# Optimization experiments

Hardware: AMD Instinct MI355X
Metric: run time of the kernel (lower is better)

The kernel has to match this reference:

```python
import jax, jax.numpy as jnp
import numpy as np

N_NODES = 50000
N_EDGES = 800000
D_IN = 128
D_OUT = 128


def setup_inputs() -> dict:
    key = jax.random.key(0)
    k1, k2, k3, k4, k5 = jax.random.split(key, 5)
    x = jax.random.normal(k1, (N_NODES, D_IN), dtype=jnp.float32)
    edge_index = jax.random.randint(k2, (2, N_EDGES), 0, N_NODES, dtype=jnp.int64)
    # PyG SAGEConv params: lin_l (neighbors, with bias), lin_r (root, no bias)
    scale = 1.0 / np.sqrt(D_IN)
    W_l = jax.random.uniform(k3, (D_OUT, D_IN), dtype=jnp.float32, minval=-scale, maxval=scale)
    b_l = jax.random.uniform(k4, (D_OUT,), dtype=jnp.float32, minval=-scale, maxval=scale)
    W_r = jax.random.uniform(k5, (D_OUT, D_IN), dtype=jnp.float32, minval=-scale, maxval=scale)
    return {"x": x, "edge_index": edge_index, "W_l": W_l, "b_l": b_l, "W_r": W_r}


def reference(x, edge_index, W_l, b_l, W_r):
    src, dst = edge_index[0], edge_index[1]
    # mean aggregation of neighbor (source) features into destination nodes
    msg = x[src]  # [E, D_IN]
    agg_sum = jax.ops.segment_sum(msg, dst, num_segments=N_NODES)  # [N, D_IN]
    deg = jax.ops.segment_sum(jnp.ones((N_EDGES,), dtype=x.dtype), dst, num_segments=N_NODES)
    agg = agg_sum / jnp.maximum(deg, 1.0)[:, None]  # isolated nodes -> 0
    # out = lin_l(agg) + lin_r(x); ReLU from SAGE_NET wrapper (active=True)
    out = agg @ W_l.T + b_l + x @ W_r.T
    return jax.nn.relu(out)
```

## Files before the change

### kernel.cpp

```cpp
#include <hip/hip_runtime.h>
#include <hip/hip_bf16.h>

#define NNODES 50000
#define NEDGES 800000
#define DD 128
#define NPART 8
#define PSIZE 6250
#define CAP 64
#define FILL_B 25000
#define XCV_B 6250
#define WB_B 64
#define WP2 68

typedef unsigned int u32;
typedef unsigned short u16;
typedef short bf16x8 __attribute__((ext_vector_type(8)));
typedef float f32x4 __attribute__((ext_vector_type(4)));
typedef float f32x2 __attribute__((ext_vector_type(2)));

#if defined(__has_builtin)
#if __has_builtin(__builtin_amdgcn_cvt_pk_f32_fp8)
#define HAVE_HW_FP8 1
#endif
#endif

union U4B8 {
    uint4 u;
    bf16x8 b;
};

__device__ __forceinline__ u32 f2b(float f) {
    u32 u = __float_as_uint(f);
    u32 rounding = 0x7fffu + ((u >> 16) & 1u);
    return (u + rounding) >> 16;
}

__device__ __forceinline__ u32 f2e4m3(float f) {
    u32 u = __float_as_uint(f);
    u32 s = (u >> 31) << 7;
    u32 mag = u & 0x7fffffffu;
    if (mag < 0x3c800000u) return s;
    u32 t = mag + 0x0007FFFFu + ((mag >> 20) & 1u);
    u32 e = (t >> 23) - 120u;
    u32 m = (t >> 20) & 7u;
    if (e > 15u || (e == 15u && m == 7u)) { e = 15u; m = 6u; }
    return s | (e << 3) | m;
}

__device__ __forceinline__ void fp8x4_acc(u32 v, float& a0, float& a1,
                                          float& a2, float& a3) {
#ifdef HAVE_HW_FP8
    f32x2 lo = __builtin_amdgcn_cvt_pk_f32_fp8((int)v, false);
    f32x2 hi = __builtin_amdgcn_cvt_pk_f32_fp8((int)v, true);
    a0 += lo.x;
    a1 += lo.y;
    a2 += hi.x;
    a3 += hi.y;
#else
#pragma unroll
    for (int b = 0; b < 4; ++b) {
        u32 byte = (v >> (8 * b)) & 0xffu;
        u32 f = ((byte >> 7) << 31) | ((((byte >> 3) & 15u) + 120u) << 23) |
                ((byte & 7u) << 20);
        float val = (byte & 0x78u) ? __uint_as_float(f) : 0.f;
        if (b == 0) a0 += val;
        else if (b == 1) a1 += val;
        else if (b == 2) a2 += val;
        else a3 += val;
    }
#endif
}

__global__ __launch_bounds__(256) void work_k(
    const int* __restrict__ ei, u32* __restrict__ deg,
    u16* __restrict__ slots16, const float* __restrict__ x,
    u32* __restrict__ xb, u32* __restrict__ xq,
    const float* __restrict__ Wl, const float* __restrict__ Wr,
    u32* __restrict__ wb) {
    const int b = blockIdx.x, tid = threadIdx.x;
    if (b < FILL_B) {
        u32 part = (u32)b & (NPART - 1);
        u32 e = ((u32)b >> 3) * 256u + tid;
        int dst = ei[NEDGES + e];
        if ((u32)(dst - part * PSIZE) < (u32)PSIZE) {
            u32 pos = atomicAdd(deg + dst, 1u);
            if (pos < CAP) slots16[(size_t)dst * CAP + pos] = (u16)ei[e];
        }
    } else if (b < FILL_B + XCV_B) {
        int i = (b - FILL_B) * 256 + tid;
        float4 v = ((const float4*)x)[i];
        uint2 o;
        o.x = f2b(v.x) | (f2b(v.y) << 16);
        o.y = f2b(v.z) | (f2b(v.w) << 16);
        ((uint2*)xb)[i] = o;
        xq[i] = f2e4m3(v.x) | (f2e4m3(v.y) << 8) | (f2e4m3(v.z) << 16) |
                (f2e4m3(v.w) << 24);
    } else {
        int idx = (b - FILL_B - XCV_B) * 256 + tid;
        int o = idx >> 7, c = idx & 127, k0 = 2 * c;
        const float* src = (k0 < DD) ? (Wl + o * DD + k0) : (Wr + o * DD + (k0 - DD));
        wb[idx] = f2b(src[0]) | (f2b(src[1]) << 16);
    }
}

__global__ __launch_bounds__(512, 4) void sage_fused_k(
    const u32* __restrict__ xq, const u16* __restrict__ slots16,
    const u32* __restrict__ deg, const u32* __restrict__ xb,
    const u32* __restrict__ wb, const float* __restrict__ bl,
    float* __restrict__ out) {
    __shared__ u32 w2[DD * WP2];
    __shared__ u32 agg_lds[128 * WP2];
    __shared__ float sbias[DD];
    const int tid = threadIdx.x;
    const int row0 = blockIdx.x * 128;
    const int wave = tid >> 6, lane = tid & 63;
    const int m = lane & 15, quad = lane >> 4;

    for (int r = tid >> 5; r < DD; r += 16) {
        int c2 = (tid & 31) * 2;
        *(uint2*)&w2[r * WP2 + c2] = *(const uint2*)&wb[r * DD + c2];
    }
    if (tid < DD) sbias[tid] = bl[tid];

    uint4 af_x[4];
    {
        int r = row0 + wave * 16 + m;
        r = r < NNODES ? r : NNODES - 1;
        const u32* xrow = xb + (size_t)r * 64;
#pragma unroll
        for (int ks = 0; ks < 4; ++ks)
            af_x[ks] = *(const uint4*)&xrow[ks * 16 + quad * 4];
    }

    const u32 half = lane >> 5;
    const u32 q = lane & 31u;
    const u32 nbase = (u32)(row0 + wave * 16);
    u32 d = (nbase < NNODES) ? deg[nbase] : 0u;
    u32 sv = (nbase < NNODES) ? (u32)slots16[(size_t)nbase * CAP + lane] : 0u;
    for (int i = 0; i < 16; ++i) {
        u32 d_n = 0u, sv_n = 0u;
        if (i < 15) {
            u32 nn = nbase + (u32)i + 1u;
            if (nn < NNODES) {
                d_n = deg[nn];
                sv_n = (u32)slots16[(size_t)nn * CAP + lane];
            }
        }
        u32 cnt = min(d, (u32)CAP);
        float a0 = 0.f, a1 = 0.f, a2 = 0.f, a3 = 0.f;
        u32 j = 0;
        for (; j + 16 <= cnt; j += 16) {
            u32 v[8];
#pragma unroll
            for (int p = 0; p < 8; ++p) {
                u32 sA = __shfl(sv, (int)(j + 2 * p), 64);
                u32 sB = __shfl(sv, (int)(j + 2 * p + 1), 64);
                u32 s = half ? sB : sA;
                v[p] = xq[(size_t)s * 32 + q];
            }
#pragma unroll
            for (int p = 0; p < 8; ++p) fp8x4_acc(v[p], a0, a1, a2, a3);
        }
        for (; j + 2 <= cnt; j += 2) {
            u32 sA = __shfl(sv, (int)j, 64);
            u32 sB = __shfl(sv, (int)(j + 1), 64);
            u32 s = half ? sB : sA;
            fp8x4_acc(xq[(size_t)s * 32 + q], a0, a1, a2, a3);
        }
        if (j < cnt) {
            u32 sA = __shfl(sv, (int)j, 64);
            u32 v = xq[(size_t)sA * 32 + q];
            if (!half) fp8x4_acc(v, a0, a1, a2, a3);
        }
        a0 += __shfl_xor(a0, 32, 64);
        a1 += __shfl_xor(a1, 32, 64);
        a2 += __shfl_xor(a2, 32, 64);
        a3 += __shfl_xor(a3, 32, 64);
        if (lane < 32) {
            float inv = 1.0f / fmaxf((float)d, 1.0f);
            uint2 o;
            o.x = f2b(a0 * inv) | (f2b(a1 * inv) << 16);
            o.y = f2b(a2 * inv) | (f2b(a3 * inv) << 16);
            *(uint2*)&agg_lds[(wave * 16 + i) * WP2 + q * 2] = o;
        }
        d = d_n;
        sv = sv_n;
    }
    __syncthreads();

    f32x4 acc[8];
#pragma unroll
    for (int nt = 0; nt < 8; ++nt) acc[nt] = (f32x4){0.f, 0.f, 0.f, 0.f};

#pragma unroll
    for (int ks = 0; ks < 4; ++ks) {
        U4B8 af;
        af.u = *(const uint4*)&agg_lds[(wave * 16 + m) * WP2 + ks * 16 + quad * 4];
#pragma unroll
        for (int nt = 0; nt < 8; ++nt) {
            U4B8 bf;
            bf.u = *(const uint4*)&w2[(nt * 16 + m) * WP2 + ks * 16 + quad * 4];
            acc[nt] = __builtin_amdgcn_mfma_f32_16x16x32_bf16(af.b, bf.b,
                                                              acc[nt], 0, 0, 0);
        }
    }
    __syncthreads();
    for (int r = tid >> 5; r < DD; r += 16) {
        int c2 = (tid & 31) * 2;
        *(uint2*)&w2[r * WP2 + c2] = *(const uint2*)&wb[r * DD + 64 + c2];
    }
    __syncthreads();

#pragma unroll
    for (int ks = 0; ks < 4; ++ks) {
        U4B8 af;
        af.u = af_x[ks];
#pragma unroll
        for (int nt = 0; nt < 8; ++nt) {
            U4B8 bf;
            bf.u = *(const uint4*)&w2[(nt * 16 + m) * WP2 + ks * 16 + quad * 4];
            acc[nt] = __builtin_amdgcn_mfma_f32_16x16x32_bf16(af.b, bf.b,
                                                              acc[nt], 0, 0, 0);
        }
    }

#pragma unroll
    for (int nt = 0; nt < 8; ++nt) {
        int col = nt * 16 + m;
        float b = sbias[col];
#pragma unroll
        for (int r_ = 0; r_ < 4; ++r_) {
            int row = row0 + wave * 16 + quad * 4 + r_;
            if (row < NNODES)
                out[(size_t)row * DD + col] = fmaxf(acc[nt][r_] + b, 0.f);
        }
    }
}

__global__ __launch_bounds__(256) void scatter_k(
    const float* __restrict__ x, const int* __restrict__ ei,
    float* __restrict__ agg, u32* __restrict__ deg) {
    u32 gid = blockIdx.x * 256u + threadIdx.x;
    u32 edge = gid >> 6;
    u32 lane = gid & 63u;
    if (edge >= NEDGES) return;
    int src = ei[edge];
    int dst = ei[NEDGES + edge];
    float2 v = ((const float2*)(x + (size_t)src * DD))[lane];
    float* p = agg + (size_t)dst * DD + lane * 2u;
    unsafeAtomicAdd(p, v.x);
    unsafeAtomicAdd(p + 1, v.y);
    if (lane == 0) atomicAdd(deg + dst, 1u);
}

__global__ __launch_bounds__(256) void mean_k(
    float* __restrict__ agg, const u32* __restrict__ deg) {
    u32 gid = blockIdx.x * 256u + threadIdx.x;
    u32 node = gid >> 6;
    u32 lane = gid & 63u;
    if (node >= NNODES) return;
    float inv = 1.0f / fmaxf((float)deg[node], 1.0f);
    float2* p = (float2*)(agg + (size_t)node * DD) + lane;
    float2 v = *p;
    *p = make_float2(v.x * inv, v.y * inv);
}

__global__ __launch_bounds__(256) void lin_l_k(
    float* __restrict__ agg,
    const float* __restrict__ Wl, const float* __restrict__ bl) {
    __shared__ u32 WT[DD * 65];
    __shared__ float rows[4 * DD];
    __shared__ float sbias[DD];
    const int tid = threadIdx.x;
    {
        u16* WTs = (u16*)WT;
        for (int i = tid; i < DD * DD; i += 256) {
            int o = i >> 7, k = i & 127;
            WTs[k * 130 + o] = (u16)f2b(Wl[i]);
        }
        if (tid < DD) sbias[tid] = bl[tid];
    }
    __syncthreads();
    const int h = tid & 63;
    const int nl = tid >> 6;
    for (int base = blockIdx.x * 4; base < NNODES; base += gridDim.x * 4) {
        ((float2*)rows)[tid] =
            ((const float2*)(agg + (size_t)(base + (tid >> 6)) * DD))[tid & 63];
        __syncthreads();
        float acc0 = sbias[2 * h], acc1 = sbias[2 * h + 1];
#pragma unroll
        for (int k = 0; k < DD; ++k) {
            float a = rows[nl * DD + k];
            u32 w2 = WT[k * 65 + h];
            acc0 = fmaf(a, __uint_as_float(w2 << 16), acc0);
            acc1 = fmaf(a, __uint_as_float(w2 & 0xffff0000u), acc1);
        }
        __syncthreads();
        ((float2*)(agg + (size_t)(base + nl) * DD))[h] = make_float2(acc0, acc1);
    }
}

__global__ __launch_bounds__(256) void lin_r_k(
    float* __restrict__ io, const float* __restrict__ x,
    const float* __restrict__ Wr) {
    __shared__ u32 WT[DD * 65];
    __shared__ float rows[4 * DD];
    const int tid = threadIdx.x;
    {
        u16* WTs = (u16*)WT;
        for (int i = tid; i < DD * DD; i += 256) {
            int o = i >> 7, k = i & 127;
            WTs[k * 130 + o] = (u16)f2b(Wr[i]);
        }
    }
    __syncthreads();
    const int h = tid & 63;
    const int nl = tid >> 6;
    for (int base = blockIdx.x * 4; base < NNODES; base += gridDim.x * 4) {
        ((float2*)rows)[tid] =
            ((const float2*)(x + (size_t)(base + (tid >> 6)) * DD))[tid & 63];
        __syncthreads();
        float2 t2 = ((const float2*)(io + (size_t)(base + nl) * DD))[h];
        float acc0 = t2.x, acc1 = t2.y;
#pragma unroll
        for (int k = 0; k < DD; ++k) {
            float a = rows[nl * DD + k];
            u32 w2 = WT[k * 65 + h];
            acc0 = fmaf(a, __uint_as_float(w2 << 16), acc0);
            acc1 = fmaf(a, __uint_as_float(w2 & 0xffff0000u), acc1);
        }
        acc0 = fmaxf(acc0, 0.f);
        acc1 = fmaxf(acc1, 0.f);
        __syncthreads();
        ((float2*)(io + (size_t)(base + nl) * DD))[h] = make_float2(acc0, acc1);
    }
}

extern "C" void kernel_launch(void* const* d_in, const int* in_sizes, int n_in,
                              void* d_out, int out_size, void* d_ws, size_t ws_size,
                              hipStream_t stream) {
    const float* x  = (const float*)d_in[0];
    const int*   ei = (const int*)d_in[1];
    const float* Wl = (const float*)d_in[2];
    const float* bl = (const float*)d_in[3];
    const float* Wr = (const float*)d_in[4];

    u32* deg     = (u32*)d_ws;
    u16* slots16 = (u16*)(deg + NNODES);
    u32* wb      = (u32*)d_ws + NNODES + (size_t)NNODES * (CAP / 2);
    u32* xb      = wb + 16384;
    u32* xq      = xb + (size_t)NNODES * 64;
    const size_t need =
        ((size_t)NNODES * (1 + CAP / 2 + 64 + 32) + 16384) * 4;

    if (ws_size >= need) {
        hipMemsetAsync(deg, 0, (size_t)NNODES * sizeof(u32), stream);
        work_k<<<FILL_B + XCV_B + WB_B, 256, 0, stream>>>(
            ei, deg, slots16, x, xb, xq, Wl, Wr, wb);
        sage_fused_k<<<(NNODES + 127) / 128, 512, 0, stream>>>(
            xq, slots16, deg, xb, wb, bl, (float*)d_out);
    } else {
        float* agg = (float*)d_out;
        hipMemsetAsync(d_out, 0, (size_t)NNODES * DD * sizeof(float), stream);
        hipMemsetAsync(d_ws, 0, (size_t)NNODES * sizeof(u32), stream);
        scatter_k<<<(NEDGES * 64) / 256, 256, 0, stream>>>(x, ei, agg, deg);
        mean_k<<<(NNODES * 64 + 255) / 256, 256, 0, stream>>>(agg, deg);
        lin_l_k<<<1024, 256, 0, stream>>>(agg, Wl, bl);
        lin_r_k<<<1024, 256, 0, stream>>>(agg, x, Wr);
    }
}
```

Measured before the change: 177.4 us.

## Interleave fill and convert blocks and halve rows per fused block

```diff
diff --git a/kernel.cpp b/kernel.cpp
--- a/kernel.cpp
+++ b/kernel.cpp
@@ -7,9 +7,8 @@
 #define NPART 8
 #define PSIZE 6250
 #define CAP 64
-#define FILL_B 25000
-#define XCV_B 6250
-#define WB_B 64
+#define NGROUPS 3910
+#define WK_B (NGROUPS * 8 + 64)
 #define WP2 68
 
 typedef unsigned int u32;
@@ -78,43 +77,54 @@
     const float* __restrict__ Wl, const float* __restrict__ Wr,
     u32* __restrict__ wb) {
     const int b = blockIdx.x, tid = threadIdx.x;
-    if (b < FILL_B) {
-        u32 part = (u32)b & (NPART - 1);
-        u32 e = ((u32)b >> 3) * 256u + tid;
-        int dst = ei[NEDGES + e];
-        if ((u32)(dst - part * PSIZE) < (u32)PSIZE) {
-            u32 pos = atomicAdd(deg + dst, 1u);
-            if (pos < CAP) slots16[(size_t)dst * CAP + pos] = (u16)ei[e];
-        }
-    } else if (b < FILL_B + XCV_B) {
-        int i = (b - FILL_B) * 256 + tid;
-        float4 v = ((const float4*)x)[i];
-        uint2 o;
-        o.x = f2b(v.x) | (f2b(v.y) << 16);
-        o.y = f2b(v.z) | (f2b(v.w) << 16);
-        ((uint2*)xb)[i] = o;
-        xq[i] = f2e4m3(v.x) | (f2e4m3(v.y) << 8) | (f2e4m3(v.z) << 16) |
-                (f2e4m3(v.w) << 24);
+    if (b < NGROUPS * 8) {
+        const u32 g = (u32)b >> 3, r8 = (u32)b & 7u;
+        const u32 gm = g % 5u, gq = g / 5u;
+        if (gm < 4u) {
+            u32 fg = gq * 4u + gm;
+            if (fg < 3125u) {
+                u32 e = fg * 256u + tid;
+                int dst = ei[NEDGES + e];
+                if ((u32)(dst - r8 * PSIZE) < (u32)PSIZE) {
+                    u32 pos = atomicAdd(deg + dst, 1u);
+                    if (pos < CAP) slots16[(size_t)dst * CAP + pos] = (u16)ei[e];
+                }
+            }
+        } else {
+            u32 xi = gq * 8u + r8;
+            if (xi < 6250u) {
+                int i = (int)xi * 256 + tid;
+                float4 v = ((const float4*)x)[i];
+                uint2 o;
+                o.x = f2b(v.x) | (f2b(v.y) << 16);
+                o.y = f2b(v.z) | (f2b(v.w) << 16);
+                ((uint2*)xb)[i] = o;
+                xq[i] = f2e4m3(v.x) | (f2e4m3(v.y) << 8) | (f2e4m3(v.z) << 16) |
+                        (f2e4m3(v.w) << 24);
+            }
+        }
     } else {
-        int idx = (b - FILL_B - XCV_B) * 256 + tid;
+        int idx = (b - NGROUPS * 8) * 256 + tid;
         int o = idx >> 7, c = idx & 127, k0 = 2 * c;
         const float* src = (k0 < DD) ? (Wl + o * DD + k0) : (Wr + o * DD + (k0 - DD));
         wb[idx] = f2b(src[0]) | (f2b(src[1]) << 16);
     }
 }
 
-__global__ __launch_bounds__(512, 4) void sage_fused_k(
+__global__ __launch_bounds__(512, 6) void sage_fused_k(
     const u32* __restrict__ xq, const u16* __restrict__ slots16,
     const u32* __restrict__ deg, const u32* __restrict__ xb,
     const u32* __restrict__ wb, const float* __restrict__ bl,
     float* __restrict__ out) {
     __shared__ u32 w2[DD * WP2];
-    __shared__ u32 agg_lds[128 * WP2];
+    __shared__ u32 agg_lds[64 * WP2];
     __shared__ float sbias[DD];
     const int tid = threadIdx.x;
-    const int row0 = blockIdx.x * 128;
+    const int row0 = blockIdx.x * 64;
     const int wave = tid >> 6, lane = tid & 63;
     const int m = lane & 15, quad = lane >> 4;
+    const int rw = wave & 3;
+    const int ch = wave >> 2;
 
     for (int r = tid >> 5; r < DD; r += 16) {
         int c2 = (tid & 31) * 2;
@@ -124,7 +134,7 @@
 
     uint4 af_x[4];
     {
-        int r = row0 + wave * 16 + m;
+        int r = row0 + rw * 16 + m;
         r = r < NNODES ? r : NNODES - 1;
         const u32* xrow = xb + (size_t)r * 64;
 #pragma unroll
@@ -134,12 +144,12 @@
 
     const u32 half = lane >> 5;
     const u32 q = lane & 31u;
-    const u32 nbase = (u32)(row0 + wave * 16);
+    const u32 nbase = (u32)(row0 + wave * 8);
     u32 d = (nbase < NNODES) ? deg[nbase] : 0u;
     u32 sv = (nbase < NNODES) ? (u32)slots16[(size_t)nbase * CAP + lane] : 0u;
-    for (int i = 0; i < 16; ++i) {
+    for (int i = 0; i < 8; ++i) {
         u32 d_n = 0u, sv_n = 0u;
-        if (i < 15) {
+        if (i < 7) {
             u32 nn = nbase + (u32)i + 1u;
             if (nn < NNODES) {
                 d_n = deg[nn];
@@ -181,25 +191,26 @@
             uint2 o;
             o.x = f2b(a0 * inv) | (f2b(a1 * inv) << 16);
             o.y = f2b(a2 * inv) | (f2b(a3 * inv) << 16);
-            *(uint2*)&agg_lds[(wave * 16 + i) * WP2 + q * 2] = o;
+            *(uint2*)&agg_lds[(wave * 8 + i) * WP2 + q * 2] = o;
         }
         d = d_n;
         sv = sv_n;
     }
     __syncthreads();
 
-    f32x4 acc[8];
-#pragma unroll
-    for (int nt = 0; nt < 8; ++nt) acc[nt] = (f32x4){0.f, 0.f, 0.f, 0.f};
+    f32x4 acc[4];
+#pragma unroll
+    for (int nt = 0; nt < 4; ++nt) acc[nt] = (f32x4){0.f, 0.f, 0.f, 0.f};
 
 #pragma unroll
     for (int ks = 0; ks < 4; ++ks) {
         U4B8 af;
-        af.u = *(const uint4*)&agg_lds[(wave * 16 + m) * WP2 + ks * 16 + quad * 4];
-#pragma unroll
-        for (int nt = 0; nt < 8; ++nt) {
+        af.u = *(const uint4*)&agg_lds[(rw * 16 + m) * WP2 + ks * 16 + quad * 4];
+#pragma unroll
+        for (int nt = 0; nt < 4; ++nt) {
             U4B8 bf;
-            bf.u = *(const uint4*)&w2[(nt * 16 + m) * WP2 + ks * 16 + quad * 4];
+            bf.u = *(const uint4*)&w2[((ch * 4 + nt) * 16 + m) * WP2 + ks * 16 +
+                                      quad * 4];
             acc[nt] = __builtin_amdgcn_mfma_f32_16x16x32_bf16(af.b, bf.b,
                                                               acc[nt], 0, 0, 0);
         }
@@ -216,21 +227,22 @@
         U4B8 af;
         af.u = af_x[ks];
 #pragma unroll
-        for (int nt = 0; nt < 8; ++nt) {
+        for (int nt = 0; nt < 4; ++nt) {
             U4B8 bf;
-            bf.u = *(const uint4*)&w2[(nt * 16 + m) * WP2 + ks * 16 + quad * 4];
+            bf.u = *(const uint4*)&w2[((ch * 4 + nt) * 16 + m) * WP2 + ks * 16 +
+                                      quad * 4];
             acc[nt] = __builtin_amdgcn_mfma_f32_16x16x32_bf16(af.b, bf.b,
                                                               acc[nt], 0, 0, 0);
         }
     }
 
 #pragma unroll
-    for (int nt = 0; nt < 8; ++nt) {
-        int col = nt * 16 + m;
+    for (int nt = 0; nt < 4; ++nt) {
+        int col = (ch * 4 + nt) * 16 + m;
         float b = sbias[col];
 #pragma unroll
         for (int r_ = 0; r_ < 4; ++r_) {
-            int row = row0 + wave * 16 + quad * 4 + r_;
+            int row = row0 + rw * 16 + quad * 4 + r_;
             if (row < NNODES)
                 out[(size_t)row * DD + col] = fmaxf(acc[nt][r_] + b, 0.f);
         }
@@ -355,9 +367,9 @@
 
     if (ws_size >= need) {
         hipMemsetAsync(deg, 0, (size_t)NNODES * sizeof(u32), stream);
-        work_k<<<FILL_B + XCV_B + WB_B, 256, 0, stream>>>(
+        work_k<<<WK_B, 256, 0, stream>>>(
             ei, deg, slots16, x, xb, xq, Wl, Wr, wb);
-        sage_fused_k<<<(NNODES + 127) / 128, 512, 0, stream>>>(
+        sage_fused_k<<<(NNODES + 63) / 64, 512, 0, stream>>>(
             xq, slots16, deg, xb, wb, bl, (float*)d_out);
     } else {
         float* agg = (float*)d_out;
```

After: 178.0 us. No clear change (+0.4%).
